# Performance work log

Hardware: AMD Instinct MI355X
Metric: run time of the kernel (lower is better)

Reference implementation:

```python
import jax, jax.numpy as jnp
import numpy as np

B, IN, OUT = 8192, 4096, 4096


def setup_inputs() -> dict:
    key = jax.random.key(0)
    k_x, k_w, k_t, k_n = jax.random.split(key, 4)
    # int8 activations and weights (stored as int8; accumulated in int32)
    x = jax.random.randint(k_x, (B, IN), -128, 128, dtype=jnp.int32).astype(jnp.int8)
    W = jax.random.randint(k_w, (OUT, IN), -128, 128, dtype=jnp.int32).astype(jnp.int8)
    # per-channel BN fold: additive term t (int32) and negative bitshift n
    t = jax.random.randint(k_t, (OUT,), -(1 << 15), 1 << 15, dtype=jnp.int32)
    n = jax.random.randint(k_n, (OUT,), -9, -6, dtype=jnp.int32)  # shift right by 6..8
    act_min = jnp.full((OUT,), -128, dtype=jnp.int32)
    act_max = jnp.full((OUT,), 127, dtype=jnp.int32)
    return {"x": x, "W": W, "t": t, "n": n, "act_min": act_min, "act_max": act_max}


def reference(x, W, t, n, act_min, act_max):
    # int32-accumulate int8 GEMM: F.linear(x, W) -> [B, OUT]
    acc = jnp.matmul(x.astype(jnp.int32), W.astype(jnp.int32).T)
    acc = acc + t  # broadcast per-output-channel bias add
    acc = jnp.right_shift(acc, -n)  # arithmetic right shift requantization
    acc = jnp.clip(acc, act_min, act_max)
    # pure_positive is False (act_min < 0) -> cast to small signed type
    return acc.astype(jnp.int8)
```

## Files before the change

kernel.cpp:

```cpp
#include <hip/hip_runtime.h>
#include <stdint.h>


#define BDIM 8192
#define INDIM 4096
#define OUTDIM 4096

typedef __attribute__((ext_vector_type(4))) int I4;
typedef __attribute__((ext_vector_type(16))) int I16;

__global__ __launch_bounds__(256) void pack_lds(const int* __restrict__ x,
                                                const int* __restrict__ W,
                                                uint32_t* __restrict__ xp,
                                                uint32_t* __restrict__ wp) {
    __shared__ uint32_t sb[8192];
    const int tid = threadIdx.x;
    const int bid = blockIdx.x;
    const int* src;
    uint32_t* dst;
    if (bid < 1024) {
        const int m32 = bid >> 2, q = bid & 3;
        src = x + (size_t)m32 * 32 * INDIM + q * 1024;
        dst = xp + (size_t)m32 * 32768 + q * 8192;
    } else {
        const int v = bid - 1024;
        const int n32 = v >> 2, q = v & 3;
        src = W + (size_t)n32 * 32 * INDIM + q * 1024;
        dst = wp + (size_t)n32 * 32768 + q * 8192;
    }
    const int kb_l = tid >> 3;
    const int lane_hi = ((tid >> 2) & 1) << 5;
    const int bslot = tid & 3;
#pragma unroll 4
    for (int rr = 0; rr < 32; ++rr) {
        int4 a = *(const int4*)(src + (size_t)rr * INDIM + tid * 4);
        uint32_t v = ((uint32_t)a.x & 255u) | (((uint32_t)a.y & 255u) << 8)
                   | (((uint32_t)a.z & 255u) << 16) | (((uint32_t)a.w & 255u) << 24);
        uint32_t idx = (uint32_t)(kb_l * 256 + (rr + lane_hi) * 4 + bslot);
        idx ^= ((idx >> 8) & 7u) << 2;
        sb[idx] = v;
    }
    __syncthreads();
#pragma unroll
    for (int it = 0; it < 8; ++it) {
        uint32_t idx = (uint32_t)(it * 1024 + tid * 4);
        idx ^= ((idx >> 8) & 7u) << 2;
        uint4 vv = *(const uint4*)&sb[idx];
        *(uint4*)(dst + it * 1024 + tid * 4) = vv;
    }
}

__device__ __forceinline__ void glds16(const void* g, void* l) {
    __builtin_amdgcn_global_load_lds((__attribute__((address_space(1))) void*)g,
                                     (__attribute__((address_space(3))) void*)l,
                                     16, 0, 0);
}

#define VMW4() asm volatile("s_waitcnt vmcnt(4)" ::: "memory")
#define VMW2() asm volatile("s_waitcnt vmcnt(2)" ::: "memory")
#define VMW0() asm volatile("s_waitcnt vmcnt(0)" ::: "memory")
#define LGKM0() asm volatile("s_waitcnt lgkmcnt(0)" ::: "memory")
#define BARRIER()                          \
    do {                                   \
        __builtin_amdgcn_s_barrier();      \
        asm volatile("" ::: "memory");     \
    } while (0)
#define SCHEDB() __builtin_amdgcn_sched_barrier(0)

#define STAGE(SETK, BUF)                                                          \
    do {                                                                          \
        _Pragma("unroll")                                                         \
        for (int i_ = 0; i_ < 2; ++i_)                                            \
            glds16(gsrc[i_] + (size_t)(SETK) * 1024,                              \
                   lds_raw + (BUF) * 16384 + (w * 2 + i_) * 1024);                \
    } while (0)

#define FRAG_READ(FA, FB, BUF)                                                    \
    do {                                                                          \
        const uint8_t* lb_ = lds_raw + (BUF) * 16384 + lane * 16;                 \
        _Pragma("unroll")                                                         \
        for (int i_ = 0; i_ < 4; ++i_)                                            \
            FA[i_] = *(const I4*)(lb_ + (wr4 + i_) * 1024);                       \
        _Pragma("unroll")                                                         \
        for (int j_ = 0; j_ < 2; ++j_)                                            \
            FB[j_] = *(const I4*)(lb_ + 8192 + (wc2 + j_) * 1024);                \
    } while (0)

#define MFMA_SET(FA, FB)                                                          \
    do {                                                                          \
        __builtin_amdgcn_s_setprio(1);                                            \
        _Pragma("unroll")                                                         \
        for (int i_ = 0; i_ < 4; ++i_)                                            \
            _Pragma("unroll")                                                     \
            for (int j_ = 0; j_ < 2; ++j_)                                        \
                acc[i_][j_] = __builtin_amdgcn_mfma_i32_32x32x32_i8(              \
                    FA[i_], FB[j_], acc[i_][j_], 0, 0, 0);                        \
        __builtin_amdgcn_s_setprio(0);                                            \
    } while (0)

#define PHASE_S(KSET, BUF, SBUF, VMW_STMT)                                        \
    do {                                                                          \
        FRAG_READ(af, bf, BUF);                                                   \
        STAGE((KSET) + 3, SBUF);                                                  \
        BARRIER();                                                                \
        LGKM0();                                                                  \
        SCHEDB();                                                                 \
        MFMA_SET(af, bf);                                                         \
        SCHEDB();                                                                 \
        VMW_STMT;                                                                 \
        BARRIER();                                                                \
    } while (0)

#define PHASE_N(BUF, VMW_STMT)                                                    \
    do {                                                                          \
        FRAG_READ(af, bf, BUF);                                                   \
        BARRIER();                                                                \
        LGKM0();                                                                  \
        SCHEDB();                                                                 \
        MFMA_SET(af, bf);                                                         \
        SCHEDB();                                                                 \
        VMW_STMT;                                                                 \
        BARRIER();                                                                \
    } while (0)

__global__ __launch_bounds__(512, 2) void gemm_lds(
    const uint8_t* __restrict__ Xp,
    const uint8_t* __restrict__ Wp,
    const int* __restrict__ t, const int* __restrict__ nsh,
    const int* __restrict__ amin, const int* __restrict__ amax,
    int* __restrict__ out) {

    const int bn = blockIdx.x;
    const int bm = blockIdx.y;
    const int tid = threadIdx.x;
    const int lane = tid & 63;
    const int w = tid >> 6;
    const int wr = w >> 2;
    const int wc = w & 3;
    const int wr4 = wr * 4;
    const int wc2 = wc * 2;

    __shared__ uint8_t lds_raw[65536];

    const uint8_t* gsrc[2];
#pragma unroll
    for (int i = 0; i < 2; ++i) {
        const int s = w * 2 + i;
        gsrc[i] = (s < 8) ? Xp + ((size_t)(bm * 8 + s) << 17) + lane * 16
                          : Wp + ((size_t)(bn * 8 + (s - 8)) << 17) + lane * 16;
    }

    I16 acc[4][2];
#pragma unroll
    for (int i = 0; i < 4; ++i)
#pragma unroll
        for (int j = 0; j < 2; ++j)
#pragma unroll
            for (int r = 0; r < 16; ++r) acc[i][j][r] = 0;

    I4 af[4], bf[2];

    STAGE(0, 0);
    STAGE(1, 1);
    STAGE(2, 2);
    VMW4();
    BARRIER();

#pragma unroll 1
    for (int kk = 0; kk < 124; kk += 4) {
        PHASE_S(kk + 0, 0, 3, VMW4());
        PHASE_S(kk + 1, 1, 0, VMW4());
        PHASE_S(kk + 2, 2, 1, VMW4());
        PHASE_S(kk + 3, 3, 2, VMW4());
    }
    PHASE_S(124, 0, 3, VMW4());
    PHASE_N(1, VMW2());
    PHASE_N(2, VMW0());
    FRAG_READ(af, bf, 3);
    LGKM0();
    SCHEDB();
    MFMA_SET(af, bf);

#pragma unroll
    for (int j = 0; j < 2; ++j) {
        const int o = bn * 256 + wc2 * 32 + j * 32 + (lane & 31);
        const int tt = t[o];
        const int sh = -nsh[o];
        const int mn = amin[o];
        const int mx = amax[o];
#pragma unroll
        for (int i = 0; i < 4; ++i) {
            const int rowbase = bm * 256 + wr4 * 32 + i * 32 + 4 * (lane >> 5);
#pragma unroll
            for (int r = 0; r < 16; ++r) {
                const int row = rowbase + (r & 3) + 8 * (r >> 2);
                int v = acc[i][j][r] + tt;
                v >>= sh;
                v = v < mn ? mn : (v > mx ? mx : v);
                __builtin_nontemporal_store(v, &out[(size_t)row * OUTDIM + o]);
            }
        }
    }
}

extern "C" void kernel_launch(void* const* d_in, const int* in_sizes, int n_in,
                              void* d_out, int out_size, void* d_ws, size_t ws_size,
                              hipStream_t stream) {
    const int* x = (const int*)d_in[0];
    const int* W = (const int*)d_in[1];
    const int* t = (const int*)d_in[2];
    const int* n = (const int*)d_in[3];
    const int* amin = (const int*)d_in[4];
    const int* amax = (const int*)d_in[5];
    int* out = (int*)d_out;

    uint8_t* xp = (uint8_t*)d_ws;
    uint8_t* wp = xp + (size_t)BDIM * INDIM;

    pack_lds<<<1536, 256, 0, stream>>>(x, W, (uint32_t*)xp, (uint32_t*)wp);

    dim3 grid(OUTDIM / 256, BDIM / 256);
    gemm_lds<<<grid, 512, 0, stream>>>(xp, wp, t, n, amin, amax, out);
}
```

Measured before the change: 393.9 us.

## Deepen LDS ring to six stages and double-buffer register fragments

Expands the global-to-LDS prefetch ring from four to six stages, so loads run further ahead. Fragment reads are double-buffered in registers: the next stage's fragments load while MFMAs run on the current ones, with one barrier per phase. The aim is to hide LDS read latency and global load latency behind the matrix math. LDS per block grows to 96KB, which likely prevents two blocks per CU and cuts occupancy, and the extra fragment registers add register pressure.

```diff
diff --git a/kernel.cpp b/kernel.cpp
--- a/kernel.cpp
+++ b/kernel.cpp
@@ -56,6 +56,8 @@
                                      16, 0, 0);
 }
 
+#define VMW8() asm volatile("s_waitcnt vmcnt(8)" ::: "memory")
+#define VMW6() asm volatile("s_waitcnt vmcnt(6)" ::: "memory")
 #define VMW4() asm volatile("s_waitcnt vmcnt(4)" ::: "memory")
 #define VMW2() asm volatile("s_waitcnt vmcnt(2)" ::: "memory")
 #define VMW0() asm volatile("s_waitcnt vmcnt(0)" ::: "memory")
@@ -98,29 +100,23 @@
         __builtin_amdgcn_s_setprio(0);                                            \
     } while (0)
 
-#define PHASE_S(KSET, BUF, SBUF, VMW_STMT)                                        \
-    do {                                                                          \
-        FRAG_READ(af, bf, BUF);                                                   \
-        STAGE((KSET) + 3, SBUF);                                                  \
-        BARRIER();                                                                \
-        LGKM0();                                                                  \
-        SCHEDB();                                                                 \
-        MFMA_SET(af, bf);                                                         \
-        SCHEDB();                                                                 \
+#define PH_S(VMW_STMT, SSET, SBUF, RBUF, RA, RB, MA, MB)                          \
+    do {                                                                          \
         VMW_STMT;                                                                 \
         BARRIER();                                                                \
-    } while (0)
-
-#define PHASE_N(BUF, VMW_STMT)                                                    \
-    do {                                                                          \
-        FRAG_READ(af, bf, BUF);                                                   \
-        BARRIER();                                                                \
-        LGKM0();                                                                  \
+        STAGE(SSET, SBUF);                                                        \
+        FRAG_READ(RA, RB, RBUF);                                                  \
+        MFMA_SET(MA, MB);                                                         \
         SCHEDB();                                                                 \
-        MFMA_SET(af, bf);                                                         \
-        SCHEDB();                                                                 \
+    } while (0)
+
+#define PH_N(VMW_STMT, RBUF, RA, RB, MA, MB)                                      \
+    do {                                                                          \
         VMW_STMT;                                                                 \
         BARRIER();                                                                \
+        FRAG_READ(RA, RB, RBUF);                                                  \
+        MFMA_SET(MA, MB);                                                         \
+        SCHEDB();                                                                 \
     } while (0)
 
 __global__ __launch_bounds__(512, 2) void gemm_lds(
@@ -140,7 +136,7 @@
     const int wr4 = wr * 4;
     const int wc2 = wc * 2;
 
-    __shared__ uint8_t lds_raw[65536];
+    __shared__ uint8_t lds_raw[98304];
 
     const uint8_t* gsrc[2];
 #pragma unroll
@@ -158,28 +154,36 @@
 #pragma unroll
             for (int r = 0; r < 16; ++r) acc[i][j][r] = 0;
 
-    I4 af[4], bf[2];
+    I4 a0[4], b0[2], a1[4], b1[2];
 
     STAGE(0, 0);
     STAGE(1, 1);
     STAGE(2, 2);
-    VMW4();
+    STAGE(3, 3);
+    STAGE(4, 4);
+    VMW8();
     BARRIER();
+    FRAG_READ(a0, b0, 0);
 
 #pragma unroll 1
-    for (int kk = 0; kk < 124; kk += 4) {
-        PHASE_S(kk + 0, 0, 3, VMW4());
-        PHASE_S(kk + 1, 1, 0, VMW4());
-        PHASE_S(kk + 2, 2, 1, VMW4());
-        PHASE_S(kk + 3, 3, 2, VMW4());
-    }
-    PHASE_S(124, 0, 3, VMW4());
-    PHASE_N(1, VMW2());
-    PHASE_N(2, VMW0());
-    FRAG_READ(af, bf, 3);
+    for (int kk = 0; kk < 120; kk += 6) {
+        PH_S(VMW6(), kk + 5, 5, 1, a1, b1, a0, b0);
+        PH_S(VMW6(), kk + 6, 0, 2, a0, b0, a1, b1);
+        PH_S(VMW6(), kk + 7, 1, 3, a1, b1, a0, b0);
+        PH_S(VMW6(), kk + 8, 2, 4, a0, b0, a1, b1);
+        PH_S(VMW6(), kk + 9, 3, 5, a1, b1, a0, b0);
+        PH_S(VMW6(), kk + 10, 4, 0, a0, b0, a1, b1);
+    }
+    PH_S(VMW6(), 125, 5, 1, a1, b1, a0, b0);
+    PH_S(VMW6(), 126, 0, 2, a0, b0, a1, b1);
+    PH_S(VMW6(), 127, 1, 3, a1, b1, a0, b0);
+    PH_N(VMW6(), 4, a0, b0, a1, b1);
+    PH_N(VMW4(), 5, a1, b1, a0, b0);
+    PH_N(VMW2(), 0, a0, b0, a1, b1);
+    PH_N(VMW0(), 1, a1, b1, a0, b0);
     LGKM0();
     SCHEDB();
-    MFMA_SET(af, bf);
+    MFMA_SET(a1, b1);
 
 #pragma unroll
     for (int j = 0; j < 2; ++j) {
```

Measured after the change: 396.4 us. No clear change (+0.6%).

## Load B fragments directly to registers and deepen A-only LDS pipeline

Applied to the files above, without the earlier changes.

Each wave now loads its two W fragments straight from global memory into registers with inline-asm global_load_dwordx4, rotating through three register buffers. Only X tiles are staged through LDS, and LDS goes from four 16KB stages to six 8KB A-only stages. The loop is restructured so that LDS fragment reads for the next step are issued alongside the MFMAs of the current step, software-pipelining LDS latency and dropping the explicit lgkmcnt waits. This removes LDS traffic and bank pressure for B, at the cost of more VGPRs. It also relies on manually tuned vmcnt counts and compiler-inserted lgkm waits being correct.

```diff
diff --git a/kernel.cpp b/kernel.cpp
--- a/kernel.cpp
+++ b/kernel.cpp
@@ -56,10 +56,9 @@
                                      16, 0, 0);
 }
 
-#define VMW4() asm volatile("s_waitcnt vmcnt(4)" ::: "memory")
+#define VMW3() asm volatile("s_waitcnt vmcnt(3)" ::: "memory")
 #define VMW2() asm volatile("s_waitcnt vmcnt(2)" ::: "memory")
 #define VMW0() asm volatile("s_waitcnt vmcnt(0)" ::: "memory")
-#define LGKM0() asm volatile("s_waitcnt lgkmcnt(0)" ::: "memory")
 #define BARRIER()                          \
     do {                                   \
         __builtin_amdgcn_s_barrier();      \
@@ -67,23 +66,25 @@
     } while (0)
 #define SCHEDB() __builtin_amdgcn_sched_barrier(0)
 
-#define STAGE(SETK, BUF)                                                          \
-    do {                                                                          \
-        _Pragma("unroll")                                                         \
-        for (int i_ = 0; i_ < 2; ++i_)                                            \
-            glds16(gsrc[i_] + (size_t)(SETK) * 1024,                              \
-                   lds_raw + (BUF) * 16384 + (w * 2 + i_) * 1024);                \
-    } while (0)
-
-#define FRAG_READ(FA, FB, BUF)                                                    \
-    do {                                                                          \
-        const uint8_t* lb_ = lds_raw + (BUF) * 16384 + lane * 16;                 \
+#define STAGE_A(SETK, BUF) \
+    glds16(ga + (size_t)(SETK) * 1024, lds_raw + (BUF) * 8192 + w * 1024)
+
+#define LOADB(SETK, LB)                                                           \
+    do {                                                                          \
+        const uint8_t* p0_ = gb0 + (size_t)(SETK) * 1024;                         \
+        const uint8_t* p1_ = gb1 + (size_t)(SETK) * 1024;                         \
+        asm volatile("global_load_dwordx4 %0, %1, off"                            \
+                     : "=&v"(LB[0]) : "v"(p0_));                                  \
+        asm volatile("global_load_dwordx4 %0, %1, off"                            \
+                     : "=&v"(LB[1]) : "v"(p1_));                                  \
+    } while (0)
+
+#define FRAG_READA(FA, BUF)                                                       \
+    do {                                                                          \
+        const uint8_t* lb_ = lds_raw + (BUF) * 8192 + lane * 16;                  \
         _Pragma("unroll")                                                         \
         for (int i_ = 0; i_ < 4; ++i_)                                            \
             FA[i_] = *(const I4*)(lb_ + (wr4 + i_) * 1024);                       \
-        _Pragma("unroll")                                                         \
-        for (int j_ = 0; j_ < 2; ++j_)                                            \
-            FB[j_] = *(const I4*)(lb_ + 8192 + (wc2 + j_) * 1024);                \
     } while (0)
 
 #define MFMA_SET(FA, FB)                                                          \
@@ -98,29 +99,25 @@
         __builtin_amdgcn_s_setprio(0);                                            \
     } while (0)
 
-#define PHASE_S(KSET, BUF, SBUF, VMW_STMT)                                        \
-    do {                                                                          \
-        FRAG_READ(af, bf, BUF);                                                   \
-        STAGE((KSET) + 3, SBUF);                                                  \
-        BARRIER();                                                                \
-        LGKM0();                                                                  \
-        SCHEDB();                                                                 \
-        MFMA_SET(af, bf);                                                         \
-        SCHEDB();                                                                 \
+#define PH_FULL(VMW_STMT, SSET, SBUF, LSET, LB, RBUF, RAF, MAF, MB)               \
+    do {                                                                          \
         VMW_STMT;                                                                 \
         BARRIER();                                                                \
-    } while (0)
-
-#define PHASE_N(BUF, VMW_STMT)                                                    \
-    do {                                                                          \
-        FRAG_READ(af, bf, BUF);                                                   \
-        BARRIER();                                                                \
-        LGKM0();                                                                  \
         SCHEDB();                                                                 \
-        MFMA_SET(af, bf);                                                         \
-        SCHEDB();                                                                 \
+        STAGE_A(SSET, SBUF);                                                      \
+        LOADB(LSET, LB);                                                          \
+        FRAG_READA(RAF, RBUF);                                                    \
+        MFMA_SET(MAF, MB);                                                        \
+    } while (0)
+
+#define PH_NOSTAGE(VMW_STMT, LSET, LB, RBUF, RAF, MAF, MB)                        \
+    do {                                                                          \
         VMW_STMT;                                                                 \
         BARRIER();                                                                \
+        SCHEDB();                                                                 \
+        LOADB(LSET, LB);                                                          \
+        FRAG_READA(RAF, RBUF);                                                    \
+        MFMA_SET(MAF, MB);                                                        \
     } while (0)
 
 __global__ __launch_bounds__(512, 2) void gemm_lds(
@@ -140,15 +137,11 @@
     const int wr4 = wr * 4;
     const int wc2 = wc * 2;
 
-    __shared__ uint8_t lds_raw[65536];
-
-    const uint8_t* gsrc[2];
-#pragma unroll
-    for (int i = 0; i < 2; ++i) {
-        const int s = w * 2 + i;
-        gsrc[i] = (s < 8) ? Xp + ((size_t)(bm * 8 + s) << 17) + lane * 16
-                          : Wp + ((size_t)(bn * 8 + (s - 8)) << 17) + lane * 16;
-    }
+    __shared__ uint8_t lds_raw[49152];
+
+    const uint8_t* ga = Xp + ((size_t)(bm * 8 + w) << 17) + lane * 16;
+    const uint8_t* gb0 = Wp + ((size_t)(bn * 8 + wc2 + 0) << 17) + lane * 16;
+    const uint8_t* gb1 = Wp + ((size_t)(bn * 8 + wc2 + 1) << 17) + lane * 16;
 
     I16 acc[4][2];
 #pragma unroll
@@ -158,28 +151,43 @@
 #pragma unroll
             for (int r = 0; r < 16; ++r) acc[i][j][r] = 0;
 
-    I4 af[4], bf[2];
-
-    STAGE(0, 0);
-    STAGE(1, 1);
-    STAGE(2, 2);
-    VMW4();
+    I4 af0[4], af1[4], b0[2], b1[2], b2[2];
+
+    STAGE_A(0, 0);
+    STAGE_A(1, 1);
+    STAGE_A(2, 2);
+    STAGE_A(3, 3);
+    LOADB(0, b0);
+    LOADB(1, b1);
+    VMW0();
     BARRIER();
+    SCHEDB();
+    FRAG_READA(af0, 0);
 
 #pragma unroll 1
-    for (int kk = 0; kk < 124; kk += 4) {
-        PHASE_S(kk + 0, 0, 3, VMW4());
-        PHASE_S(kk + 1, 1, 0, VMW4());
-        PHASE_S(kk + 2, 2, 1, VMW4());
-        PHASE_S(kk + 3, 3, 2, VMW4());
-    }
-    PHASE_S(124, 0, 3, VMW4());
-    PHASE_N(1, VMW2());
-    PHASE_N(2, VMW0());
-    FRAG_READ(af, bf, 3);
-    LGKM0();
+    for (int kk = 0; kk < 120; kk += 6) {
+        PH_FULL(VMW3(), kk + 4, 4, kk + 2, b2, 1, af1, af0, b0);
+        PH_FULL(VMW3(), kk + 5, 5, kk + 3, b0, 2, af0, af1, b1);
+        PH_FULL(VMW3(), kk + 6, 0, kk + 4, b1, 3, af1, af0, b2);
+        PH_FULL(VMW3(), kk + 7, 1, kk + 5, b2, 4, af0, af1, b0);
+        PH_FULL(VMW3(), kk + 8, 2, kk + 6, b0, 5, af1, af0, b1);
+        PH_FULL(VMW3(), kk + 9, 3, kk + 7, b1, 0, af0, af1, b2);
+    }
+    PH_FULL(VMW3(), 124, 4, 122, b2, 1, af1, af0, b0);
+    PH_FULL(VMW3(), 125, 5, 123, b0, 2, af0, af1, b1);
+    PH_FULL(VMW3(), 126, 0, 124, b1, 3, af1, af0, b2);
+    PH_FULL(VMW3(), 127, 1, 125, b2, 4, af0, af1, b0);
+    PH_NOSTAGE(VMW3(), 126, b0, 5, af1, af0, b1);
+    PH_NOSTAGE(VMW2(), 127, b1, 0, af0, af1, b2);
+    VMW2();
+    BARRIER();
     SCHEDB();
-    MFMA_SET(af, bf);
+    FRAG_READA(af1, 1);
+    MFMA_SET(af0, b0);
+    VMW0();
+    BARRIER();
+    SCHEDB();
+    MFMA_SET(af1, b1);
 
 #pragma unroll
     for (int j = 0; j < 2; ++j) {
```

Result: no change. 392.8 us (-0.3%).
